# Optimization experiments

Measured on AMD Instinct MI355X. Metric: run time of the kernel, lower is better.

The kernel has to match this reference:

```python
import jax, jax.numpy as jnp
import numpy as np

H = 2048        # hidden_size
I = 1408        # moe_intermediate_size
E = 8           # n_routed_experts
TOP_K = 2       # num_experts_per_tok
N_SHARED = 2
IS = N_SHARED * I  # shared expert intermediate


def setup_inputs() -> dict:
    key = jax.random.key(0)
    ks = jax.random.split(key, 8)
    s_h = 1.0 / np.sqrt(H)
    s_i = 1.0 / np.sqrt(I)
    s_is = 1.0 / np.sqrt(IS)
    return {
        "hidden_states": jax.random.normal(ks[0], (1, 2048, H), jnp.float32),
        "gate_w": jax.random.normal(ks[1], (E, H), jnp.float32) * s_h,
        "w_gate": jax.random.normal(ks[2], (E, H, I), jnp.float32) * s_h,
        "w_up": jax.random.normal(ks[3], (E, H, I), jnp.float32) * s_h,
        "w_down": jax.random.normal(ks[4], (E, I, H), jnp.float32) * s_i,
        "sw_gate": jax.random.normal(ks[5], (H, IS), jnp.float32) * s_h,
        "sw_up": jax.random.normal(ks[6], (H, IS), jnp.float32) * s_h,
        "sw_down": jax.random.normal(ks[7], (IS, H), jnp.float32) * s_is,
    }


def reference(hidden_states, gate_w, w_gate, w_up, w_down, sw_gate, sw_up, sw_down):
    B, S, _ = hidden_states.shape
    x = hidden_states.reshape(-1, H)          # [N, H]
    N = x.shape[0]

    # --- gate: softmax over expert logits, then top-k (DeepSeek greedy gate) ---
    logits = x @ gate_w.T                      # [N, E]
    scores = jax.nn.softmax(logits, axis=-1)
    topk_w, topk_i = jax.lax.top_k(scores, TOP_K)   # [N, K]

    # --- routed experts: dense compute per expert, masked combine ---
    g = jnp.einsum('nh,ehi->eni', x, w_gate)   # [E, N, I]
    u = jnp.einsum('nh,ehi->eni', x, w_up)
    h = jax.nn.silu(g) * u
    eo = jnp.einsum('eni,eih->enh', h, w_down)  # [E, N, H]

    # combine weights: scatter top-k softmax scores into [N, E]
    combine = jnp.zeros((N, E), x.dtype).at[jnp.arange(N)[:, None], topk_i].add(topk_w)
    y = jnp.einsum('ne,enh->nh', combine, eo)  # weighted scatter-reduce combine

    # --- shared experts (always-on SwiGLU MLP) ---
    sh = jax.nn.silu(x @ sw_gate) * (x @ sw_up)
    y = y + sh @ sw_down

    return y.reshape(B, S, H)
```

## Files before the change

kernel.cpp:

```cpp
#include <hip/hip_runtime.h>
#include <hip/hip_bf16.h>

#define H    2048
#define NI   1408
#define NE   8
#define NTOK 2048
#define NIS  2816

typedef __bf16 bf16x8 __attribute__((ext_vector_type(8)));
typedef float  f32x4  __attribute__((ext_vector_type(4)));

#define ASYNC16(gp, lp) __builtin_amdgcn_global_load_lds( \
    (const __attribute__((address_space(1))) void*)(gp),  \
    (__attribute__((address_space(3))) void*)(lp), 16, 0, 0)

__global__ __launch_bounds__(256)
void cvt_kernel(const float* __restrict__ in, __bf16* __restrict__ out)
{
    size_t i = ((size_t)blockIdx.x * 256 + threadIdx.x) * 8;
    float4 v0 = *(const float4*)(in + i);
    float4 v1 = *(const float4*)(in + i + 4);
    union { __bf16 b[8]; uint4 u; } p;
    p.b[0] = (__bf16)v0.x; p.b[1] = (__bf16)v0.y;
    p.b[2] = (__bf16)v0.z; p.b[3] = (__bf16)v0.w;
    p.b[4] = (__bf16)v1.x; p.b[5] = (__bf16)v1.y;
    p.b[6] = (__bf16)v1.z; p.b[7] = (__bf16)v1.w;
    *(uint4*)(out + i) = p.u;
}

__global__ __launch_bounds__(256)
void cvt_t_kernel(const float* __restrict__ in, __bf16* __restrict__ out,
                  int K, int N)
{
    const size_t zoff = (size_t)blockIdx.z * K * N;
    in  += zoff;
    out += zoff;
    const int n0 = blockIdx.x * 64;
    const int k0 = blockIdx.y * 64;
    __shared__ __bf16 tile[64][72];
    const int t = threadIdx.x;
    const int tr  = t >> 4;
    const int tc4 = (t & 15) * 4;
#pragma unroll
    for (int i = 0; i < 4; ++i) {
        int k = i * 16 + tr;
        float4 v = *(const float4*)(in + (size_t)(k0 + k) * N + n0 + tc4);
        tile[k][tc4 + 0] = (__bf16)v.x;
        tile[k][tc4 + 1] = (__bf16)v.y;
        tile[k][tc4 + 2] = (__bf16)v.z;
        tile[k][tc4 + 3] = (__bf16)v.w;
    }
    __syncthreads();
    const int n = t >> 2, q = t & 3;
#pragma unroll
    for (int hh = 0; hh < 2; ++hh) {
        int qq = q + hh * 4;
        union { __bf16 b[8]; uint4 u; } pk;
#pragma unroll
        for (int j = 0; j < 8; ++j) pk.b[j] = tile[qq * 8 + j][n];
        *(uint4*)(out + (size_t)(n0 + n) * K + k0 + qq * 8) = pk.u;
    }
}

__global__ __launch_bounds__(256)
void gate_kernel(const float* __restrict__ x, const float* __restrict__ gw,
                 float* __restrict__ topw, int* __restrict__ pairs,
                 int* __restrict__ cnt)
{
    int tok  = blockIdx.x * 4 + (threadIdx.x >> 6);
    int lane = threadIdx.x & 63;
    float acc[NE];
#pragma unroll
    for (int e = 0; e < NE; ++e) acc[e] = 0.f;
    const float* xr = x + (size_t)tok * H;
    for (int h = lane; h < H; h += 64) {
        float xv = xr[h];
#pragma unroll
        for (int e = 0; e < NE; ++e) acc[e] += xv * gw[e * H + h];
    }
#pragma unroll
    for (int e = 0; e < NE; ++e) {
        float v = acc[e];
        for (int off = 32; off; off >>= 1) v += __shfl_xor(v, off);
        acc[e] = v;
    }
    if (lane == 0) {
        float mx = acc[0];
#pragma unroll
        for (int e = 1; e < NE; ++e) mx = fmaxf(mx, acc[e]);
        float p[NE]; float s = 0.f;
#pragma unroll
        for (int e = 0; e < NE; ++e) { p[e] = __expf(acc[e] - mx); s += p[e]; }
        float inv = 1.f / s;
        int e1 = 0;
#pragma unroll
        for (int e = 1; e < NE; ++e) if (acc[e] > acc[e1]) e1 = e;
        int e2 = -1;
#pragma unroll
        for (int e = 0; e < NE; ++e) {
            if (e == e1) continue;
            if (e2 < 0 || acc[e] > acc[e2]) e2 = e;
        }
        topw[tok * 2 + 0] = p[e1] * inv;
        topw[tok * 2 + 1] = p[e2] * inv;
        int pos1 = atomicAdd(&cnt[e1], 1);
        pairs[e1 * NTOK + pos1] = tok * 2 + 0;
        int pos2 = atomicAdd(&cnt[e2], 1);
        pairs[e2 * NTOK + pos2] = tok * 2 + 1;
    }
}

__global__ __launch_bounds__(256, 2)
void gu_kernel(const __bf16* __restrict__ xb,
               const __bf16* __restrict__ wgT, const __bf16* __restrict__ wuT,
               const __bf16* __restrict__ swgT, const __bf16* __restrict__ swuT,
               __bf16* __restrict__ h_sh, __bf16* __restrict__ h_rt,
               const int* __restrict__ pairs, const int* __restrict__ cnt)
{
    const int t = threadIdx.x, lane = t & 63;
    const int wid = t >> 6, wm = wid >> 1, wn = wid & 1;
    const int e = blockIdx.z;
    const bool routed = (e < NE);
    const int m0 = blockIdx.y * 128, n0 = blockIdx.x * 128;

    int count = NTOK;
    const __bf16 *Bg, *Bu;
    __bf16* outp;
    int ldO;
    if (routed) {
        if (n0 >= NI) return;
        count = cnt[e];
        if (m0 >= count) return;
        Bg = wgT + (size_t)e * NI * H;
        Bu = wuT + (size_t)e * NI * H;
        outp = h_rt; ldO = NI;
    } else {
        Bg = swgT; Bu = swuT; outp = h_sh; ldO = NIS;
    }

    __shared__ __align__(16) __bf16 At[128 * 32], Btg[128 * 32], Btu[128 * 32];
    __shared__ int tile_pid[128];
    if (t < 128) {
        int j = m0 + t;
        tile_pid[t] = routed ? ((j < count) ? pairs[e * NTOK + j] : -1) : j;
    }
    __syncthreads();

    const int r = t >> 2, c = t & 3;
    size_t ar0, ar1;
    if (routed) {
        int p0 = tile_pid[r];      if (p0 < 0) p0 = 0;
        int p1 = tile_pid[r + 64]; if (p1 < 0) p1 = 0;
        ar0 = (size_t)(p0 >> 1); ar1 = (size_t)(p1 >> 1);
    } else {
        ar0 = (size_t)(m0 + r); ar1 = (size_t)(m0 + r + 64);
    }
    const __bf16* a0 = xb + ar0 * H + c * 8;
    const __bf16* a1 = xb + ar1 * H + c * 8;
    const __bf16* g0 = Bg + (size_t)(n0 + r) * H + c * 8;
    const __bf16* g1 = Bg + (size_t)(n0 + r + 64) * H + c * 8;
    const __bf16* u0 = Bu + (size_t)(n0 + r) * H + c * 8;
    const __bf16* u1 = Bu + (size_t)(n0 + r + 64) * H + c * 8;
    __bf16* lA0 = At  + t * 8;  __bf16* lA1 = At  + (256 + t) * 8;
    __bf16* lG0 = Btg + t * 8;  __bf16* lG1 = Btg + (256 + t) * 8;
    __bf16* lU0 = Btu + t * 8;  __bf16* lU1 = Btu + (256 + t) * 8;

    f32x4 accg[4][4] = {};
    f32x4 accu[4][4] = {};

    for (int k0 = 0; k0 < H; k0 += 32) {
        __syncthreads();
        ASYNC16(a0 + k0, lA0); ASYNC16(a1 + k0, lA1);
        ASYNC16(g0 + k0, lG0); ASYNC16(g1 + k0, lG1);
        ASYNC16(u0 + k0, lU0); ASYNC16(u1 + k0, lU1);
        __syncthreads();
        bf16x8 a[4];
#pragma unroll
        for (int mi = 0; mi < 4; ++mi)
            a[mi] = *(const bf16x8*)(At + (wm * 64 + mi * 16 + (lane & 15)) * 32 + (lane >> 4) * 8);
#pragma unroll
        for (int ni = 0; ni < 4; ++ni) {
            bf16x8 bg = *(const bf16x8*)(Btg + (wn * 64 + ni * 16 + (lane & 15)) * 32 + (lane >> 4) * 8);
            bf16x8 bu = *(const bf16x8*)(Btu + (wn * 64 + ni * 16 + (lane & 15)) * 32 + (lane >> 4) * 8);
#pragma unroll
            for (int mi = 0; mi < 4; ++mi) {
                accg[mi][ni] = __builtin_amdgcn_mfma_f32_16x16x32_bf16(a[mi], bg, accg[mi][ni], 0, 0, 0);
                accu[mi][ni] = __builtin_amdgcn_mfma_f32_16x16x32_bf16(a[mi], bu, accu[mi][ni], 0, 0, 0);
            }
        }
    }

#pragma unroll
    for (int mi = 0; mi < 4; ++mi) {
#pragma unroll
        for (int rr = 0; rr < 4; ++rr) {
            int row = wm * 64 + mi * 16 + (lane >> 4) * 4 + rr;
            int pid = tile_pid[row];
            if (routed && pid < 0) continue;
            size_t orow = routed ? (size_t)pid : (size_t)(m0 + row);
#pragma unroll
            for (int ni = 0; ni < 4; ++ni) {
                int col = n0 + wn * 64 + ni * 16 + (lane & 15);
                float g = accg[mi][ni][rr];
                float u = accu[mi][ni][rr];
                float hv = g / (1.f + __expf(-g)) * u;
                outp[orow * (size_t)ldO + col] = (__bf16)hv;
            }
        }
    }
}

__global__ __launch_bounds__(256, 2)
void down_kernel(const __bf16* __restrict__ h_sh, const __bf16* __restrict__ h_rt,
                 const __bf16* __restrict__ swdT, const __bf16* __restrict__ wdT,
                 float* __restrict__ out,
                 const int* __restrict__ pairs, const int* __restrict__ cnt,
                 const float* __restrict__ topw)
{
    const int t = threadIdx.x, lane = t & 63;
    const int wid = t >> 6, wm = wid >> 1, wn = wid & 1;
    const int e = blockIdx.z;
    const bool routed = (e < NE);
    const int m0 = blockIdx.y * 128, n0 = blockIdx.x * 128;

    int count = NTOK, K, lda, koff = 0;
    const __bf16 *A, *B;
    if (routed) {
        count = cnt[e];
        if (m0 >= count) return;
        A = h_rt; lda = NI; K = NI;
        B = wdT + (size_t)e * H * NI;
    } else {
        A = h_sh; lda = NIS; K = NI;
        koff = (e == NE) ? 0 : NI;
        B = swdT;
    }

    __shared__ __align__(16) __bf16 At[128 * 32], Bt[128 * 32];
    __shared__ int tile_pid[128];
    if (t < 128) {
        int j = m0 + t;
        tile_pid[t] = routed ? ((j < count) ? pairs[e * NTOK + j] : -1) : j;
    }
    __syncthreads();

    const int r = t >> 2, c = t & 3;
    size_t ar0, ar1;
    if (routed) {
        int p0 = tile_pid[r];      if (p0 < 0) p0 = 0;
        int p1 = tile_pid[r + 64]; if (p1 < 0) p1 = 0;
        ar0 = (size_t)p0; ar1 = (size_t)p1;
    } else {
        ar0 = (size_t)(m0 + r); ar1 = (size_t)(m0 + r + 64);
    }
    const __bf16* a0 = A + ar0 * lda + koff + c * 8;
    const __bf16* a1 = A + ar1 * lda + koff + c * 8;
    const __bf16* b0 = B + (size_t)(n0 + r) * lda + koff + c * 8;
    const __bf16* b1 = B + (size_t)(n0 + r + 64) * lda + koff + c * 8;
    __bf16* lA0 = At + t * 8;  __bf16* lA1 = At + (256 + t) * 8;
    __bf16* lB0 = Bt + t * 8;  __bf16* lB1 = Bt + (256 + t) * 8;

    f32x4 acc[4][4] = {};

    for (int k0 = 0; k0 < K; k0 += 32) {
        __syncthreads();
        ASYNC16(a0 + k0, lA0); ASYNC16(a1 + k0, lA1);
        ASYNC16(b0 + k0, lB0); ASYNC16(b1 + k0, lB1);
        __syncthreads();
        bf16x8 a[4];
#pragma unroll
        for (int mi = 0; mi < 4; ++mi)
            a[mi] = *(const bf16x8*)(At + (wm * 64 + mi * 16 + (lane & 15)) * 32 + (lane >> 4) * 8);
#pragma unroll
        for (int ni = 0; ni < 4; ++ni) {
            bf16x8 b = *(const bf16x8*)(Bt + (wn * 64 + ni * 16 + (lane & 15)) * 32 + (lane >> 4) * 8);
#pragma unroll
            for (int mi = 0; mi < 4; ++mi)
                acc[mi][ni] = __builtin_amdgcn_mfma_f32_16x16x32_bf16(a[mi], b, acc[mi][ni], 0, 0, 0);
        }
    }

#pragma unroll
    for (int mi = 0; mi < 4; ++mi) {
#pragma unroll
        for (int rr = 0; rr < 4; ++rr) {
            int row = wm * 64 + mi * 16 + (lane >> 4) * 4 + rr;
            int pid = tile_pid[row];
            if (routed && pid < 0) continue;
            size_t tok; float w;
            if (routed) { tok = (size_t)(pid >> 1); w = topw[pid]; }
            else        { tok = (size_t)(m0 + row); w = 1.f; }
#pragma unroll
            for (int ni = 0; ni < 4; ++ni) {
                int col = n0 + wn * 64 + ni * 16 + (lane & 15);
                atomicAdd(out + tok * H + col, w * acc[mi][ni][rr]);
            }
        }
    }
}

extern "C" void kernel_launch(void* const* d_in, const int* in_sizes, int n_in,
                              void* d_out, int out_size, void* d_ws, size_t ws_size,
                              hipStream_t stream)
{
    const float* x       = (const float*)d_in[0];
    const float* gate_w  = (const float*)d_in[1];
    const float* w_gate  = (const float*)d_in[2];
    const float* w_up    = (const float*)d_in[3];
    const float* w_down  = (const float*)d_in[4];
    const float* sw_gate = (const float*)d_in[5];
    const float* sw_up   = (const float*)d_in[6];
    const float* sw_down = (const float*)d_in[7];

    char*   ws    = (char*)d_ws;
    float*  topw  = (float*)ws;
    int*    cnt   = (int*)(ws + 16384);
    int*    pairs = (int*)(ws + 16512);
    __bf16* xb    = (__bf16*)(ws + 131072);
    __bf16* h_sh  = (__bf16*)(ws + 8519680);
    __bf16* h_rt  = (__bf16*)(ws + 20054016);
    __bf16* swgT  = (__bf16*)(ws + 31588352);
    __bf16* swuT  = (__bf16*)(ws + 43122688);
    __bf16* swdT  = (__bf16*)(ws + 54657024);
    __bf16* wgT   = (__bf16*)(ws + 66191360);
    __bf16* wuT   = (__bf16*)(ws + 112328704);
    __bf16* wdT   = wgT;

    hipMemsetAsync(cnt, 0, NE * sizeof(int), stream);
    hipMemsetAsync(d_out, 0, (size_t)NTOK * H * sizeof(float), stream);

    cvt_kernel<<<NTOK * H / 2048, 256, 0, stream>>>(x, xb);
    cvt_t_kernel<<<dim3(NIS / 64, H / 64, 1), 256, 0, stream>>>(sw_gate, swgT, H, NIS);
    cvt_t_kernel<<<dim3(NIS / 64, H / 64, 1), 256, 0, stream>>>(sw_up,   swuT, H, NIS);
    cvt_t_kernel<<<dim3(H / 64, NIS / 64, 1), 256, 0, stream>>>(sw_down, swdT, NIS, H);
    cvt_t_kernel<<<dim3(NI / 64, H / 64, NE), 256, 0, stream>>>(w_gate,  wgT,  H, NI);
    cvt_t_kernel<<<dim3(NI / 64, H / 64, NE), 256, 0, stream>>>(w_up,    wuT,  H, NI);

    gate_kernel<<<NTOK / 4, 256, 0, stream>>>(x, gate_w, topw, pairs, cnt);

    gu_kernel<<<dim3(NIS / 128, NTOK / 128, NE + 1), 256, 0, stream>>>(
        xb, wgT, wuT, swgT, swuT, h_sh, h_rt, pairs, cnt);

    cvt_t_kernel<<<dim3(H / 64, NI / 64, NE), 256, 0, stream>>>(w_down, wdT, NI, H);

    down_kernel<<<dim3(H / 128, NTOK / 128, NE + 2), 256, 0, stream>>>(
        h_sh, h_rt, swdT, wdT, (float*)d_out, pairs, cnt, topw);
}
```

Before: 682.8 us.

## Merge conversions into one launch and compact routed GEMM grids via a work queue

All fp32→bf16 weight and activation conversions are merged into a single segmented kernel launch. When the workspace is large enough, the w_down conversion also joins that launch instead of running between the two GEMMs. A small scheduler kernel builds a compact list of (expert, m-tile) work items from the routing counts, so the gate/up and down kernels launch a flat 1D grid without the many early-exiting empty blocks. Routed gate/up tiles shrink to 64 columns to add blocks for occupancy, at the cost of less B reuse per block and an extra serial single-thread kernel.

```diff
diff --git a/kernel.cpp b/kernel.cpp
--- a/kernel.cpp
+++ b/kernel.cpp
@@ -14,51 +14,61 @@
     (const __attribute__((address_space(1))) void*)(gp),  \
     (__attribute__((address_space(3))) void*)(lp), 16, 0, 0)
 
+struct CvtSeg {
+    const float* src; __bf16* dst;
+    int K, N, ntx, tiles_per_mat, count, trans;
+};
+struct CvtArgs { CvtSeg s[7]; int base[8]; int nseg; };
+
 __global__ __launch_bounds__(256)
-void cvt_kernel(const float* __restrict__ in, __bf16* __restrict__ out)
-{
-    size_t i = ((size_t)blockIdx.x * 256 + threadIdx.x) * 8;
-    float4 v0 = *(const float4*)(in + i);
-    float4 v1 = *(const float4*)(in + i + 4);
-    union { __bf16 b[8]; uint4 u; } p;
-    p.b[0] = (__bf16)v0.x; p.b[1] = (__bf16)v0.y;
-    p.b[2] = (__bf16)v0.z; p.b[3] = (__bf16)v0.w;
-    p.b[4] = (__bf16)v1.x; p.b[5] = (__bf16)v1.y;
-    p.b[6] = (__bf16)v1.z; p.b[7] = (__bf16)v1.w;
-    *(uint4*)(out + i) = p.u;
-}
-
-__global__ __launch_bounds__(256)
-void cvt_t_kernel(const float* __restrict__ in, __bf16* __restrict__ out,
-                  int K, int N)
-{
-    const size_t zoff = (size_t)blockIdx.z * K * N;
-    in  += zoff;
-    out += zoff;
-    const int n0 = blockIdx.x * 64;
-    const int k0 = blockIdx.y * 64;
+void cvt_all_kernel(CvtArgs a)
+{
+    const int b = blockIdx.x;
+    int si = 0;
+    while (si + 1 < a.nseg && b >= a.base[si + 1]) ++si;
+    const CvtSeg seg = a.s[si];
+    int local = b - a.base[si];
+    int mat = local / seg.tiles_per_mat;
+    int rem = local - mat * seg.tiles_per_mat;
+    int tx = rem % seg.ntx;
+    int ty = rem / seg.ntx;
+    const float* src = seg.src + (size_t)mat * seg.K * seg.N;
+    __bf16*      dst = seg.dst + (size_t)mat * seg.K * seg.N;
+    const int n0 = tx * 64, k0 = ty * 64;
+    const int t = threadIdx.x;
+    const int tr = t >> 4, tc4 = (t & 15) * 4;
+
+    if (!seg.trans) {
+#pragma unroll
+        for (int i = 0; i < 4; ++i) {
+            int k = i * 16 + tr;
+            float4 v = *(const float4*)(src + (size_t)(k0 + k) * seg.N + n0 + tc4);
+            union { __bf16 h[4]; uint2 u; } p;
+            p.h[0] = (__bf16)v.x; p.h[1] = (__bf16)v.y;
+            p.h[2] = (__bf16)v.z; p.h[3] = (__bf16)v.w;
+            *(uint2*)(dst + (size_t)(k0 + k) * seg.N + n0 + tc4) = p.u;
+        }
+        return;
+    }
     __shared__ __bf16 tile[64][72];
-    const int t = threadIdx.x;
-    const int tr  = t >> 4;
-    const int tc4 = (t & 15) * 4;
 #pragma unroll
     for (int i = 0; i < 4; ++i) {
         int k = i * 16 + tr;
-        float4 v = *(const float4*)(in + (size_t)(k0 + k) * N + n0 + tc4);
+        float4 v = *(const float4*)(src + (size_t)(k0 + k) * seg.N + n0 + tc4);
         tile[k][tc4 + 0] = (__bf16)v.x;
         tile[k][tc4 + 1] = (__bf16)v.y;
         tile[k][tc4 + 2] = (__bf16)v.z;
         tile[k][tc4 + 3] = (__bf16)v.w;
     }
     __syncthreads();
-    const int n = t >> 2, q = t & 3;
+    const int n = t >> 2, q4 = t & 3;
 #pragma unroll
     for (int hh = 0; hh < 2; ++hh) {
-        int qq = q + hh * 4;
-        union { __bf16 b[8]; uint4 u; } pk;
-#pragma unroll
-        for (int j = 0; j < 8; ++j) pk.b[j] = tile[qq * 8 + j][n];
-        *(uint4*)(out + (size_t)(n0 + n) * K + k0 + qq * 8) = pk.u;
+        int qq = q4 + hh * 4;
+        union { __bf16 h[8]; uint4 u; } pk;
+#pragma unroll
+        for (int j = 0; j < 8; ++j) pk.h[j] = tile[qq * 8 + j][n];
+        *(uint4*)(dst + (size_t)(n0 + n) * seg.K + k0 + qq * 8) = pk.u;
     }
 }
 
@@ -110,39 +120,54 @@
     }
 }
 
+__global__ void sched_kernel(const int* __restrict__ cnt, int* __restrict__ q)
+{
+    if (threadIdx.x == 0) {
+        int pos = 0;
+        for (int e = 0; e < NE; ++e) {
+            int tc = (cnt[e] + 127) >> 7;
+            for (int i = 0; i < tc; ++i) q[1 + pos++] = e | (i << 4);
+        }
+        q[0] = pos;
+    }
+}
+
 __global__ __launch_bounds__(256, 2)
 void gu_kernel(const __bf16* __restrict__ xb,
                const __bf16* __restrict__ wgT, const __bf16* __restrict__ wuT,
                const __bf16* __restrict__ swgT, const __bf16* __restrict__ swuT,
                __bf16* __restrict__ h_sh, __bf16* __restrict__ h_rt,
-               const int* __restrict__ pairs, const int* __restrict__ cnt)
+               const int* __restrict__ pairs, const int* __restrict__ cnt,
+               const int* __restrict__ q)
 {
     const int t = threadIdx.x, lane = t & 63;
     const int wid = t >> 6, wm = wid >> 1, wn = wid & 1;
-    const int e = blockIdx.z;
-    const bool routed = (e < NE);
-    const int m0 = blockIdx.y * 128, n0 = blockIdx.x * 128;
-
-    int count = NTOK;
+    const int b = blockIdx.x;
+    const bool routed = (b >= 352);
+    int e = 0, m0, n0, count;
     const __bf16 *Bg, *Bu;
-    __bf16* outp;
-    int ldO;
     if (routed) {
-        if (n0 >= NI) return;
+        int j = b - 352;
+        int p = j / 22, nt = j - p * 22;
+        if (p >= q[0]) return;
+        int item = q[1 + p];
+        e = item & 15;
+        m0 = (item >> 4) * 128;
+        n0 = nt * 64;
         count = cnt[e];
-        if (m0 >= count) return;
         Bg = wgT + (size_t)e * NI * H;
         Bu = wuT + (size_t)e * NI * H;
-        outp = h_rt; ldO = NI;
     } else {
-        Bg = swgT; Bu = swuT; outp = h_sh; ldO = NIS;
+        int mt = b / 22, nt = b - mt * 22;
+        m0 = mt * 128; n0 = nt * 128; count = NTOK;
+        Bg = swgT; Bu = swuT;
     }
 
     __shared__ __align__(16) __bf16 At[128 * 32], Btg[128 * 32], Btu[128 * 32];
     __shared__ int tile_pid[128];
     if (t < 128) {
-        int j = m0 + t;
-        tile_pid[t] = routed ? ((j < count) ? pairs[e * NTOK + j] : -1) : j;
+        int jj = m0 + t;
+        tile_pid[t] = routed ? ((jj < count) ? pairs[e * NTOK + jj] : -1) : jj;
     }
     __syncthreads();
 
@@ -158,8 +183,8 @@
     const __bf16* a0 = xb + ar0 * H + c * 8;
     const __bf16* a1 = xb + ar1 * H + c * 8;
     const __bf16* g0 = Bg + (size_t)(n0 + r) * H + c * 8;
+    const __bf16* u0 = Bu + (size_t)(n0 + r) * H + c * 8;
     const __bf16* g1 = Bg + (size_t)(n0 + r + 64) * H + c * 8;
-    const __bf16* u0 = Bu + (size_t)(n0 + r) * H + c * 8;
     const __bf16* u1 = Bu + (size_t)(n0 + r + 64) * H + c * 8;
     __bf16* lA0 = At  + t * 8;  __bf16* lA1 = At  + (256 + t) * 8;
     __bf16* lG0 = Btg + t * 8;  __bf16* lG1 = Btg + (256 + t) * 8;
@@ -171,25 +196,42 @@
     for (int k0 = 0; k0 < H; k0 += 32) {
         __syncthreads();
         ASYNC16(a0 + k0, lA0); ASYNC16(a1 + k0, lA1);
-        ASYNC16(g0 + k0, lG0); ASYNC16(g1 + k0, lG1);
-        ASYNC16(u0 + k0, lU0); ASYNC16(u1 + k0, lU1);
+        ASYNC16(g0 + k0, lG0); ASYNC16(u0 + k0, lU0);
+        if (!routed) { ASYNC16(g1 + k0, lG1); ASYNC16(u1 + k0, lU1); }
         __syncthreads();
         bf16x8 a[4];
 #pragma unroll
         for (int mi = 0; mi < 4; ++mi)
             a[mi] = *(const bf16x8*)(At + (wm * 64 + mi * 16 + (lane & 15)) * 32 + (lane >> 4) * 8);
-#pragma unroll
-        for (int ni = 0; ni < 4; ++ni) {
-            bf16x8 bg = *(const bf16x8*)(Btg + (wn * 64 + ni * 16 + (lane & 15)) * 32 + (lane >> 4) * 8);
-            bf16x8 bu = *(const bf16x8*)(Btu + (wn * 64 + ni * 16 + (lane & 15)) * 32 + (lane >> 4) * 8);
-#pragma unroll
-            for (int mi = 0; mi < 4; ++mi) {
-                accg[mi][ni] = __builtin_amdgcn_mfma_f32_16x16x32_bf16(a[mi], bg, accg[mi][ni], 0, 0, 0);
-                accu[mi][ni] = __builtin_amdgcn_mfma_f32_16x16x32_bf16(a[mi], bu, accu[mi][ni], 0, 0, 0);
+        if (routed) {
+#pragma unroll
+            for (int ni = 0; ni < 2; ++ni) {
+                bf16x8 bg = *(const bf16x8*)(Btg + (wn * 32 + ni * 16 + (lane & 15)) * 32 + (lane >> 4) * 8);
+                bf16x8 bu = *(const bf16x8*)(Btu + (wn * 32 + ni * 16 + (lane & 15)) * 32 + (lane >> 4) * 8);
+#pragma unroll
+                for (int mi = 0; mi < 4; ++mi) {
+                    accg[mi][ni] = __builtin_amdgcn_mfma_f32_16x16x32_bf16(a[mi], bg, accg[mi][ni], 0, 0, 0);
+                    accu[mi][ni] = __builtin_amdgcn_mfma_f32_16x16x32_bf16(a[mi], bu, accu[mi][ni], 0, 0, 0);
+                }
             }
-        }
-    }
-
+        } else {
+#pragma unroll
+            for (int ni = 0; ni < 4; ++ni) {
+                bf16x8 bg = *(const bf16x8*)(Btg + (wn * 64 + ni * 16 + (lane & 15)) * 32 + (lane >> 4) * 8);
+                bf16x8 bu = *(const bf16x8*)(Btu + (wn * 64 + ni * 16 + (lane & 15)) * 32 + (lane >> 4) * 8);
+#pragma unroll
+                for (int mi = 0; mi < 4; ++mi) {
+                    accg[mi][ni] = __builtin_amdgcn_mfma_f32_16x16x32_bf16(a[mi], bg, accg[mi][ni], 0, 0, 0);
+                    accu[mi][ni] = __builtin_amdgcn_mfma_f32_16x16x32_bf16(a[mi], bu, accu[mi][ni], 0, 0, 0);
+                }
+            }
+        }
+    }
+
+    const int nis = routed ? 2 : 4;
+    const int wnw = routed ? 32 : 64;
+    __bf16* outp = routed ? h_rt : h_sh;
+    const int ldO = routed ? NI : NIS;
 #pragma unroll
     for (int mi = 0; mi < 4; ++mi) {
 #pragma unroll
@@ -198,9 +240,8 @@
             int pid = tile_pid[row];
             if (routed && pid < 0) continue;
             size_t orow = routed ? (size_t)pid : (size_t)(m0 + row);
-#pragma unroll
-            for (int ni = 0; ni < 4; ++ni) {
-                int col = n0 + wn * 64 + ni * 16 + (lane & 15);
+            for (int ni = 0; ni < nis; ++ni) {
+                int col = n0 + wn * wnw + ni * 16 + (lane & 15);
                 float g = accg[mi][ni][rr];
                 float u = accu[mi][ni][rr];
                 float hv = g / (1.f + __expf(-g)) * u;
@@ -215,32 +256,36 @@
                  const __bf16* __restrict__ swdT, const __bf16* __restrict__ wdT,
                  float* __restrict__ out,
                  const int* __restrict__ pairs, const int* __restrict__ cnt,
-                 const float* __restrict__ topw)
+                 const float* __restrict__ topw, const int* __restrict__ q)
 {
     const int t = threadIdx.x, lane = t & 63;
     const int wid = t >> 6, wm = wid >> 1, wn = wid & 1;
-    const int e = blockIdx.z;
-    const bool routed = (e < NE);
-    const int m0 = blockIdx.y * 128, n0 = blockIdx.x * 128;
-
-    int count = NTOK, K, lda, koff = 0;
+    const int b = blockIdx.x;
+    const bool routed = (b >= 512);
+    int e = 0, m0, n0, koff = 0, count, lda;
     const __bf16 *A, *B;
     if (routed) {
+        int j = b - 512;
+        int p = j >> 4, nt = j & 15;
+        if (p >= q[0]) return;
+        int item = q[1 + p];
+        e = item & 15;
+        m0 = (item >> 4) * 128; n0 = nt * 128;
         count = cnt[e];
-        if (m0 >= count) return;
-        A = h_rt; lda = NI; K = NI;
+        A = h_rt; lda = NI;
         B = wdT + (size_t)e * H * NI;
     } else {
-        A = h_sh; lda = NIS; K = NI;
-        koff = (e == NE) ? 0 : NI;
-        B = swdT;
+        int kh = b >> 8, rem = b & 255;
+        n0 = (rem & 15) * 128; m0 = (rem >> 4) * 128;
+        koff = kh * NI; count = NTOK;
+        A = h_sh; lda = NIS; B = swdT;
     }
 
     __shared__ __align__(16) __bf16 At[128 * 32], Bt[128 * 32];
     __shared__ int tile_pid[128];
     if (t < 128) {
-        int j = m0 + t;
-        tile_pid[t] = routed ? ((j < count) ? pairs[e * NTOK + j] : -1) : j;
+        int jj = m0 + t;
+        tile_pid[t] = routed ? ((jj < count) ? pairs[e * NTOK + jj] : -1) : jj;
     }
     __syncthreads();
 
@@ -262,7 +307,7 @@
 
     f32x4 acc[4][4] = {};
 
-    for (int k0 = 0; k0 < K; k0 += 32) {
+    for (int k0 = 0; k0 < NI; k0 += 32) {
         __syncthreads();
         ASYNC16(a0 + k0, lA0); ASYNC16(a1 + k0, lA1);
         ASYNC16(b0 + k0, lB0); ASYNC16(b1 + k0, lB1);
@@ -273,10 +318,10 @@
             a[mi] = *(const bf16x8*)(At + (wm * 64 + mi * 16 + (lane & 15)) * 32 + (lane >> 4) * 8);
 #pragma unroll
         for (int ni = 0; ni < 4; ++ni) {
-            bf16x8 b = *(const bf16x8*)(Bt + (wn * 64 + ni * 16 + (lane & 15)) * 32 + (lane >> 4) * 8);
+            bf16x8 bb = *(const bf16x8*)(Bt + (wn * 64 + ni * 16 + (lane & 15)) * 32 + (lane >> 4) * 8);
 #pragma unroll
             for (int mi = 0; mi < 4; ++mi)
-                acc[mi][ni] = __builtin_amdgcn_mfma_f32_16x16x32_bf16(a[mi], b, acc[mi][ni], 0, 0, 0);
+                acc[mi][ni] = __builtin_amdgcn_mfma_f32_16x16x32_bf16(a[mi], bb, acc[mi][ni], 0, 0, 0);
         }
     }
 
@@ -297,6 +342,21 @@
             }
         }
     }
+}
+
+static void add_seg(CvtArgs& a, int& nb, const float* s, __bf16* d,
+                    int K, int N, int nmat, int trans)
+{
+    CvtSeg sg;
+    sg.src = s; sg.dst = d; sg.K = K; sg.N = N;
+    sg.ntx = N / 64;
+    sg.tiles_per_mat = (N / 64) * (K / 64);
+    sg.trans = trans;
+    sg.count = sg.tiles_per_mat * nmat;
+    a.base[a.nseg] = nb;
+    a.s[a.nseg++] = sg;
+    nb += sg.count;
+    a.base[a.nseg] = nb;
 }
 
 extern "C" void kernel_launch(void* const* d_in, const int* in_sizes, int n_in,
@@ -315,7 +375,8 @@
     char*   ws    = (char*)d_ws;
     float*  topw  = (float*)ws;
     int*    cnt   = (int*)(ws + 16384);
-    int*    pairs = (int*)(ws + 16512);
+    int*    q     = (int*)(ws + 16512);
+    int*    pairs = (int*)(ws + 17408);
     __bf16* xb    = (__bf16*)(ws + 131072);
     __bf16* h_sh  = (__bf16*)(ws + 8519680);
     __bf16* h_rt  = (__bf16*)(ws + 20054016);
@@ -324,25 +385,34 @@
     __bf16* swdT  = (__bf16*)(ws + 54657024);
     __bf16* wgT   = (__bf16*)(ws + 66191360);
     __bf16* wuT   = (__bf16*)(ws + 112328704);
-    __bf16* wdT   = wgT;
+    const bool bigws = ws_size >= (size_t)158466048 + 46137344;
+    __bf16* wdT   = bigws ? (__bf16*)(ws + 158466048) : wgT;
 
     hipMemsetAsync(cnt, 0, NE * sizeof(int), stream);
     hipMemsetAsync(d_out, 0, (size_t)NTOK * H * sizeof(float), stream);
 
-    cvt_kernel<<<NTOK * H / 2048, 256, 0, stream>>>(x, xb);
-    cvt_t_kernel<<<dim3(NIS / 64, H / 64, 1), 256, 0, stream>>>(sw_gate, swgT, H, NIS);
-    cvt_t_kernel<<<dim3(NIS / 64, H / 64, 1), 256, 0, stream>>>(sw_up,   swuT, H, NIS);
-    cvt_t_kernel<<<dim3(H / 64, NIS / 64, 1), 256, 0, stream>>>(sw_down, swdT, NIS, H);
-    cvt_t_kernel<<<dim3(NI / 64, H / 64, NE), 256, 0, stream>>>(w_gate,  wgT,  H, NI);
-    cvt_t_kernel<<<dim3(NI / 64, H / 64, NE), 256, 0, stream>>>(w_up,    wuT,  H, NI);
-
     gate_kernel<<<NTOK / 4, 256, 0, stream>>>(x, gate_w, topw, pairs, cnt);
-
-    gu_kernel<<<dim3(NIS / 128, NTOK / 128, NE + 1), 256, 0, stream>>>(
-        xb, wgT, wuT, swgT, swuT, h_sh, h_rt, pairs, cnt);
-
-    cvt_t_kernel<<<dim3(H / 64, NI / 64, NE), 256, 0, stream>>>(w_down, wdT, NI, H);
-
-    down_kernel<<<dim3(H / 128, NTOK / 128, NE + 2), 256, 0, stream>>>(
-        h_sh, h_rt, swdT, wdT, (float*)d_out, pairs, cnt, topw);
-}
+    sched_kernel<<<1, 64, 0, stream>>>(cnt, q);
+
+    CvtArgs ca; ca.nseg = 0; int nb = 0;
+    add_seg(ca, nb, x,       xb,   NTOK, H,  1,  0);
+    add_seg(ca, nb, sw_gate, swgT, H,  NIS,  1,  1);
+    add_seg(ca, nb, sw_up,   swuT, H,  NIS,  1,  1);
+    add_seg(ca, nb, sw_down, swdT, NIS, H,   1,  1);
+    add_seg(ca, nb, w_gate,  wgT,  H,  NI,   NE, 1);
+    add_seg(ca, nb, w_up,    wuT,  H,  NI,   NE, 1);
+    if (bigws) add_seg(ca, nb, w_down, wdT, NI, H, NE, 1);
+    cvt_all_kernel<<<nb, 256, 0, stream>>>(ca);
+
+    gu_kernel<<<352 + 22 * 40, 256, 0, stream>>>(
+        xb, wgT, wuT, swgT, swuT, h_sh, h_rt, pairs, cnt, q);
+
+    if (!bigws) {
+        CvtArgs cb; cb.nseg = 0; int nb2 = 0;
+        add_seg(cb, nb2, w_down, wdT, NI, H, NE, 1);
+        cvt_all_kernel<<<nb2, 256, 0, stream>>>(cb);
+    }
+
+    down_kernel<<<512 + 16 * 40, 256, 0, stream>>>(
+        h_sh, h_rt, swdT, wdT, (float*)d_out, pairs, cnt, topw, q);
+}
```

Result: slower. 2.547 ms (+273.0%).
